# Kernel optimization log

Measured on AMD Instinct MI355X. Metric: run time of the kernel, lower is better.

Reference implementation:

```python
import jax, jax.numpy as jnp
import numpy as np

TAU = 2.0        # LIF membrane time constant
VTH = 1.0        # firing threshold
ALPHA = 2.0      # ATan surrogate sharpness (spikingjelly default)
EPS = 1e-5       # LayerNorm eps


@jax.custom_vjp
def spike(x):
    # Heaviside forward, ATan surrogate backward (spikingjelly surrogate.ATan)
    return (x >= 0).astype(x.dtype)

def _spike_fwd(x):
    return (x >= 0).astype(x.dtype), x

def _spike_bwd(x, g):
    return (g * (ALPHA / 2.0) / (1.0 + (jnp.pi / 2.0 * ALPHA * x) ** 2),)

spike.defvjp(_spike_fwd, _spike_bwd)


def lif(x_tbd):
    """Multi-step LIF neuron, decay_input=True, hard reset v_reset=0, detach_reset=True.
    x_tbd: [T, B, D] -> spikes [T, B, D]."""
    def step(v, x):
        v = v + (x - v) / TAU                       # leaky integrate
        s = spike(v - VTH)                          # fire
        v = v * (1.0 - jax.lax.stop_gradient(s))    # detached hard reset to 0
        return v, s
    v0 = jnp.zeros(x_tbd.shape[1:], x_tbd.dtype)
    _, s = jax.lax.scan(step, v0, x_tbd)
    return s


def layernorm(x, g, b):
    m = x.mean(-1, keepdims=True)
    v = ((x - m) ** 2).mean(-1, keepdims=True)
    return (x - m) * jax.lax.rsqrt(v + EPS) * g + b


def setup_inputs() -> dict:
    key = jax.random.key(0)
    ks = jax.random.split(key, 8)
    B, T, IN, H0, D, HD, DEPTH = 64, 2048, 4, 64, 128, 256, 4
    def w(k, shape, fan_in):
        return jax.random.normal(k, shape, jnp.float32) * (1.0 / np.sqrt(fan_in))
    return {
        "hist_feat": jax.random.normal(ks[0], (B, T, IN), jnp.float32),
        # projector params
        "pw1": w(ks[1], (IN, H0), IN), "pb1": jnp.zeros((H0,), jnp.float32),
        "pw2": w(ks[2], (H0, D), H0), "pb2": jnp.zeros((D,), jnp.float32),
        # stacked block params [DEPTH, ...]
        "fc1_w": w(ks[3], (DEPTH, D, HD), D), "fc1_b": jnp.zeros((DEPTH, HD), jnp.float32),
        "n1_g": jnp.ones((DEPTH, HD), jnp.float32), "n1_b": jnp.zeros((DEPTH, HD), jnp.float32),
        "fc2_w": w(ks[4], (DEPTH, HD, D), HD), "fc2_b": jnp.zeros((DEPTH, D), jnp.float32),
        "n2_g": jnp.ones((DEPTH, D), jnp.float32), "n2_b": jnp.zeros((DEPTH, D), jnp.float32),
    }


def reference(hist_feat, pw1, pb1, pw2, pb2, fc1_w, fc1_b, n1_g, n1_b,
              fc2_w, fc2_b, n2_g, n2_b):
    # SpikeInputProjector: Linear -> exact GELU -> Linear
    x = jax.nn.gelu(hist_feat @ pw1 + pb1, approximate=False) @ pw2 + pb2  # [B,T,D]
    depth = fc1_w.shape[0]
    for i in range(depth):  # small fixed structural loop over blocks
        r = x
        h = layernorm(x @ fc1_w[i] + fc1_b[i], n1_g[i], n1_b[i])   # [B,T,HD]
        h = lif(h.swapaxes(0, 1)).swapaxes(0, 1)                    # LIF over time
        h = layernorm(h @ fc2_w[i] + fc2_b[i], n2_g[i], n2_b[i])   # [B,T,D]
        h = lif(h.swapaxes(0, 1)).swapaxes(0, 1)
        x = r + h
    return x[:, -1]  # pooling='last', mask=None
```

## Files before the change

kernel.cpp:

```cpp
#include <hip/hip_runtime.h>
#include <math.h>

#define NB   64
#define TT   2048
#define TW   64
#define T0   (TT - TW)
#define NR   (NB * TW)

typedef float v2f __attribute__((ext_vector_type(2)));

__device__ __forceinline__ float gelu_exact(float x) {
    return 0.5f * x * (1.0f + erff(x * 0.7071067811865476f));
}
__device__ __forceinline__ unsigned long long rfl64(unsigned long long x) {
    unsigned lo = __builtin_amdgcn_readfirstlane((unsigned)x);
    unsigned hi = __builtin_amdgcn_readfirstlane((unsigned)(x >> 32));
    return ((unsigned long long)hi << 32) | lo;
}

#define XT_O   0
#define WB0_O  4096
#define WB1_O  12288
#define V1_O   20480
#define V2_O   20736
#define MSK_O  20864
#define LB_TOT 21120

__global__ void __launch_bounds__(512) fused_kernel(
    const float* __restrict__ hist,
    const float* __restrict__ pw1, const float* __restrict__ pb1,
    const float* __restrict__ pw2, const float* __restrict__ pb2,
    const float* __restrict__ fc1w, const float* __restrict__ fc1b,
    const float* __restrict__ n1g,  const float* __restrict__ n1b,
    const float* __restrict__ fc2w, const float* __restrict__ fc2b,
    const float* __restrict__ n2g,  const float* __restrict__ n2b,
    float* __restrict__ v1buf, float* __restrict__ v2buf,
    int* __restrict__ flg1, int* __restrict__ flg2,
    float* __restrict__ out)
{
    __shared__ __align__(16) float LB[LB_TOT];
    __shared__ int FLG[2];
    unsigned long long* MSK = (unsigned long long*)&LB[MSK_O];
    const int tid = threadIdx.x, wave = tid >> 6, lane = tid & 63;
    const int b = blockIdx.x & 63, half = blockIdx.x >> 6;
    const int row0 = wave * 4;

    if (tid == 0) { FLG[0] = 0; FLG[1] = 0; }

    float4 ra, rb, rc, rd;
#define LOADQ(src) { const float4* p_ = (const float4*)(src); \
                     ra = p_[tid]; rb = p_[tid+512]; rc = p_[tid+1024]; rd = p_[tid+1536]; }
#define WRITEQ(off) { float4* q_ = (float4*)&LB[off]; \
                      q_[tid] = ra; q_[tid+512] = rb; q_[tid+1024] = rc; q_[tid+1536] = rd; }
#define CONSUME(WOFF, KQ) \
    { \
        _Pragma("unroll 2") \
        for (int k4 = 0; k4 < 8; ++k4) { \
            float4 xr[4]; \
            _Pragma("unroll") \
            for (int r = 0; r < 4; ++r) \
                xr[r] = *(const float4*)&LB[XT_O + (row0+r)*128 + (KQ) + k4*4]; \
            _Pragma("unroll") \
            for (int kk = 0; kk < 4; ++kk) { \
                float4 wv = ((const float4*)&LB[(WOFF) + (k4*4+kk)*256])[lane]; \
                v2f wA, wB; wA.x = wv.x; wA.y = wv.y; wB.x = wv.z; wB.y = wv.w; \
                _Pragma("unroll") \
                for (int r = 0; r < 4; ++r) { \
                    float xv = ((const float*)&xr[r])[kk]; \
                    accA[r] += wA * xv; \
                    accB[r] += wB * xv; \
                } \
            } \
        } \
    }

    LOADQ(fc1w);

    {
        const float* hb = hist + ((size_t)b * TT + T0 + half*32) * 4;
        float w0 = pw1[lane], w1 = pw1[64+lane], w2 = pw1[128+lane], w3 = pw1[192+lane];
        float bb = pb1[lane];
        #pragma unroll
        for (int r = 0; r < 4; ++r) {
            int t = row0 + r;
            float4 h = *(const float4*)(hb + t*4);
            LB[WB1_O + t*64 + lane] = gelu_exact(bb + h.x*w0 + h.y*w1 + h.z*w2 + h.w*w3);
        }
    }
    WRITEQ(WB0_O);
    LOADQ(fc1w + 8192);
    {
        float2 bv = ((const float2*)pb2)[lane];
        v2f acc[4];
        #pragma unroll
        for (int r = 0; r < 4; ++r) { acc[r].x = 0.f; acc[r].y = 0.f; }
        #pragma unroll 2
        for (int k4 = 0; k4 < 16; ++k4) {
            float4 xr[4];
            #pragma unroll
            for (int r = 0; r < 4; ++r)
                xr[r] = *(const float4*)&LB[WB1_O + (row0+r)*64 + k4*4];
            #pragma unroll
            for (int kk = 0; kk < 4; ++kk) {
                v2f w = ((const v2f*)(pw2 + (k4*4+kk)*128))[lane];
                #pragma unroll
                for (int r = 0; r < 4; ++r) {
                    float xv = ((const float*)&xr[r])[kk];
                    acc[r] += w * xv;
                }
            }
        }
        #pragma unroll
        for (int r = 0; r < 4; ++r) {
            float2 o; o.x = acc[r].x + bv.x; o.y = acc[r].y + bv.y;
            *(float2*)&LB[XT_O + (row0+r)*128 + lane*2] = o;
        }
    }

    #pragma unroll 1
    for (int l = 0; l < 4; ++l) {
        const float* W1l = fc1w + (size_t)l * 32768;
        const float* W1n = fc1w + (size_t)(l < 3 ? l+1 : l) * 32768;
        const float* W2g = fc2w + (size_t)l * 32768;

        v2f accA[4], accB[4];
        #pragma unroll
        for (int r = 0; r < 4; ++r) {
            accA[r].x = 0.f; accA[r].y = 0.f;
            accB[r].x = 0.f; accB[r].y = 0.f;
        }
        __syncthreads(); WRITEQ(WB1_O); LOADQ(W1l + 16384); CONSUME(WB0_O, 0);
        __syncthreads(); WRITEQ(WB0_O); LOADQ(W1l + 24576); CONSUME(WB1_O, 32);
        __syncthreads(); WRITEQ(WB1_O); LOADQ(W1n);         CONSUME(WB0_O, 64);
        __syncthreads(); WRITEQ(WB0_O); LOADQ(W1n + 8192);  CONSUME(WB1_O, 96);

        {
            float4 b1v = ((const float4*)(fc1b + l*256))[lane];
            float4 g1v = ((const float4*)(n1g  + l*256))[lane];
            float4 t1v = ((const float4*)(n1b  + l*256))[lane];
            #pragma unroll
            for (int r = 0; r < 4; ++r) {
                float a0 = accA[r].x + b1v.x, a1 = accA[r].y + b1v.y;
                float a2 = accB[r].x + b1v.z, a3 = accB[r].y + b1v.w;
                float s = a0 + a1 + a2 + a3;
                #pragma unroll
                for (int m = 1; m < 64; m <<= 1) s += __shfl_xor(s, m, 64);
                float mean = s * (1.0f/256.0f);
                float dx = a0-mean, dy = a1-mean, dz = a2-mean, dw = a3-mean;
                float q2 = dx*dx + dy*dy + dz*dz + dw*dw;
                #pragma unroll
                for (int m = 1; m < 64; m <<= 1) q2 += __shfl_xor(q2, m, 64);
                float inv = 1.0f / sqrtf(q2 * (1.0f/256.0f) + 1e-5f);
                accA[r].x = dx*inv*g1v.x + t1v.x; accA[r].y = dy*inv*g1v.y + t1v.y;
                accB[r].x = dz*inv*g1v.z + t1v.z; accB[r].y = dw*inv*g1v.w + t1v.w;
            }
        }
        {
            const int tgt = l*8 + wave;
            while (__hip_atomic_load(&FLG[0], __ATOMIC_ACQUIRE,
                                     __HIP_MEMORY_SCOPE_WORKGROUP) < tgt)
                __builtin_amdgcn_s_sleep(1);
            float v0, v1, v2, v3;
            if (wave == 0) {
                if (half == 0) { v0 = v1 = v2 = v3 = 0.f; }
                else {
                    while (__hip_atomic_load(&flg1[b], __ATOMIC_RELAXED,
                                             __HIP_MEMORY_SCOPE_AGENT) < l+1)
                        __builtin_amdgcn_s_sleep(1);
                    __builtin_amdgcn_fence(__ATOMIC_ACQUIRE, "agent");
                    float4 vv = *(const float4*)&v1buf[(size_t)l*NB*256 + b*256 + lane*4];
                    v0 = vv.x; v1 = vv.y; v2 = vv.z; v3 = vv.w;
                }
            } else {
                float4 vv = *(const float4*)&LB[V1_O + lane*4];
                v0 = vv.x; v1 = vv.y; v2 = vv.z; v3 = vv.w;
            }
            #pragma unroll
            for (int i = 0; i < 4; ++i) {
                v0 += (accA[i].x - v0) * 0.5f;
                v1 += (accA[i].y - v1) * 0.5f;
                v2 += (accB[i].x - v2) * 0.5f;
                v3 += (accB[i].y - v3) * 0.5f;
                bool s0 = v0 >= 1.f, s1 = v1 >= 1.f, s2 = v2 >= 1.f, s3 = v3 >= 1.f;
                unsigned long long b0 = __ballot(s0), b1 = __ballot(s1);
                unsigned long long b2 = __ballot(s2), b3 = __ballot(s3);
                if (lane == 0) {
                    unsigned long long* mp = MSK + (size_t)(wave*4 + i)*4;
                    mp[0] = b0; mp[1] = b1; mp[2] = b2; mp[3] = b3;
                }
                v0 = s0 ? 0.f : v0;  v1 = s1 ? 0.f : v1;
                v2 = s2 ? 0.f : v2;  v3 = s3 ? 0.f : v3;
            }
            if (wave < 7) {
                float4 vv; vv.x = v0; vv.y = v1; vv.z = v2; vv.w = v3;
                *(float4*)&LB[V1_O + lane*4] = vv;
            } else if (half == 0) {
                float4 vv; vv.x = v0; vv.y = v1; vv.z = v2; vv.w = v3;
                *(float4*)&v1buf[(size_t)l*NB*256 + b*256 + lane*4] = vv;
                __builtin_amdgcn_fence(__ATOMIC_RELEASE, "agent");
                if (lane == 0)
                    __hip_atomic_store(&flg1[b], l+1, __ATOMIC_RELAXED,
                                       __HIP_MEMORY_SCOPE_AGENT);
            }
            if (lane == 0)
                __hip_atomic_store(&FLG[0], tgt+1, __ATOMIC_RELEASE,
                                   __HIP_MEMORY_SCOPE_WORKGROUP);
        }
        float a2x[4], a2y[4];
        #pragma unroll
        for (int i = 0; i < 4; ++i) {
            const unsigned long long* mp = MSK + (size_t)(wave*4 + i)*4;
            unsigned long long m0 = rfl64(mp[0]);
            unsigned long long m1 = rfl64(mp[1]);
            unsigned long long m2 = rfl64(mp[2]);
            unsigned long long m3 = rfl64(mp[3]);
            unsigned long long mm = m0 | m1 | m2 | m3;
            float ax = 0.f, ay = 0.f;
            if (mm) {
                int id = __builtin_ctzll(mm); mm &= mm - 1;
                const float* wr = W2g + (size_t)id * 512;
                float2 w0 = ((const float2*)(wr      ))[lane];
                float2 w1 = ((const float2*)(wr + 128))[lane];
                float2 w2 = ((const float2*)(wr + 256))[lane];
                float2 w3 = ((const float2*)(wr + 384))[lane];
                unsigned long long bit = 1ull << id;
                while (mm) {
                    int id2 = __builtin_ctzll(mm); mm &= mm - 1;
                    const float* wr2 = W2g + (size_t)id2 * 512;
                    float2 n0 = ((const float2*)(wr2      ))[lane];
                    float2 n1 = ((const float2*)(wr2 + 128))[lane];
                    float2 n2 = ((const float2*)(wr2 + 256))[lane];
                    float2 n3 = ((const float2*)(wr2 + 384))[lane];
                    ax += (m0 & bit) ? w0.x : 0.f;  ay += (m0 & bit) ? w0.y : 0.f;
                    ax += (m1 & bit) ? w1.x : 0.f;  ay += (m1 & bit) ? w1.y : 0.f;
                    ax += (m2 & bit) ? w2.x : 0.f;  ay += (m2 & bit) ? w2.y : 0.f;
                    ax += (m3 & bit) ? w3.x : 0.f;  ay += (m3 & bit) ? w3.y : 0.f;
                    bit = 1ull << id2;
                    w0 = n0; w1 = n1; w2 = n2; w3 = n3;
                }
                ax += (m0 & bit) ? w0.x : 0.f;  ay += (m0 & bit) ? w0.y : 0.f;
                ax += (m1 & bit) ? w1.x : 0.f;  ay += (m1 & bit) ? w1.y : 0.f;
                ax += (m2 & bit) ? w2.x : 0.f;  ay += (m2 & bit) ? w2.y : 0.f;
                ax += (m3 & bit) ? w3.x : 0.f;  ay += (m3 & bit) ? w3.y : 0.f;
            }
            a2x[i] = ax; a2y[i] = ay;
        }
        {
            float2 b2v = ((const float2*)(fc2b + l*128))[lane];
            float2 g2v = ((const float2*)(n2g  + l*128))[lane];
            float2 t2v = ((const float2*)(n2b  + l*128))[lane];
            #pragma unroll
            for (int i = 0; i < 4; ++i) {
                float ax = a2x[i] + b2v.x, ay = a2y[i] + b2v.y;
                float s = ax + ay;
                #pragma unroll
                for (int m = 1; m < 64; m <<= 1) s += __shfl_xor(s, m, 64);
                float mean = s * (1.0f/128.0f);
                float dx = ax - mean, dy = ay - mean;
                float q = dx*dx + dy*dy;
                #pragma unroll
                for (int m = 1; m < 64; m <<= 1) q += __shfl_xor(q, m, 64);
                float inv = 1.0f / sqrtf(q * (1.0f/128.0f) + 1e-5f);
                a2x[i] = dx*inv*g2v.x + t2v.x;
                a2y[i] = dy*inv*g2v.y + t2v.y;
            }
        }
        {
            const int tgt = l*8 + wave;
            while (__hip_atomic_load(&FLG[1], __ATOMIC_ACQUIRE,
                                     __HIP_MEMORY_SCOPE_WORKGROUP) < tgt)
                __builtin_amdgcn_s_sleep(1);
            float u0, u1;
            if (wave == 0) {
                if (half == 0) { u0 = u1 = 0.f; }
                else {
                    while (__hip_atomic_load(&flg2[b], __ATOMIC_RELAXED,
                                             __HIP_MEMORY_SCOPE_AGENT) < l+1)
                        __builtin_amdgcn_s_sleep(1);
                    __builtin_amdgcn_fence(__ATOMIC_ACQUIRE, "agent");
                    float2 uv = *(const float2*)&v2buf[(size_t)l*NB*128 + b*128 + lane*2];
                    u0 = uv.x; u1 = uv.y;
                }
            } else {
                float2 uv = *(const float2*)&LB[V2_O + lane*2];
                u0 = uv.x; u1 = uv.y;
            }
            #pragma unroll
            for (int i = 0; i < 4; ++i) {
                int t = row0 + i;
                u0 += (a2x[i] - u0) * 0.5f;
                u1 += (a2y[i] - u1) * 0.5f;
                bool s0 = u0 >= 1.f, s1 = u1 >= 1.f;
                float2 xv = *(const float2*)&LB[XT_O + t*128 + lane*2];
                float2 xn;
                xn.x = xv.x + (s0 ? 1.f : 0.f);
                xn.y = xv.y + (s1 ? 1.f : 0.f);
                *(float2*)&LB[XT_O + t*128 + lane*2] = xn;
                u0 = s0 ? 0.f : u0;
                u1 = s1 ? 0.f : u1;
                if (l == 3 && half == 1 && t == 31)
                    ((float2*)(out + b*128))[lane] = xn;
            }
            if (wave < 7) {
                float2 uv; uv.x = u0; uv.y = u1;
                *(float2*)&LB[V2_O + lane*2] = uv;
            } else if (half == 0) {
                float2 uv; uv.x = u0; uv.y = u1;
                *(float2*)&v2buf[(size_t)l*NB*128 + b*128 + lane*2] = uv;
                __builtin_amdgcn_fence(__ATOMIC_RELEASE, "agent");
                if (lane == 0)
                    __hip_atomic_store(&flg2[b], l+1, __ATOMIC_RELAXED,
                                       __HIP_MEMORY_SCOPE_AGENT);
            }
            if (lane == 0)
                __hip_atomic_store(&FLG[1], tgt+1, __ATOMIC_RELEASE,
                                   __HIP_MEMORY_SCOPE_WORKGROUP);
        }
    }
#undef LOADQ
#undef WRITEQ
#undef CONSUME
}

extern "C" void kernel_launch(void* const* d_in, const int* in_sizes, int n_in,
                              void* d_out, int out_size, void* d_ws, size_t ws_size,
                              hipStream_t stream) {
    const float* hist = (const float*)d_in[0];
    const float* pw1  = (const float*)d_in[1];
    const float* pb1  = (const float*)d_in[2];
    const float* pw2  = (const float*)d_in[3];
    const float* pb2  = (const float*)d_in[4];
    const float* fc1w = (const float*)d_in[5];
    const float* fc1b = (const float*)d_in[6];
    const float* n1g  = (const float*)d_in[7];
    const float* n1b  = (const float*)d_in[8];
    const float* fc2w = (const float*)d_in[9];
    const float* fc2b = (const float*)d_in[10];
    const float* n2g  = (const float*)d_in[11];
    const float* n2b  = (const float*)d_in[12];
    float* out = (float*)d_out;

    char* ws = (char*)d_ws;
    float* v1buf = (float*)ws;
    float* v2buf = (float*)(ws + (1ull << 20));
    int*   flg1  = (int*)(ws + (2ull << 20));
    int*   flg2  = flg1 + 64;

    hipMemsetAsync(flg1, 0, 128 * sizeof(int), stream);
    fused_kernel<<<128, 512, 0, stream>>>(hist, pw1, pb1, pw2, pb2,
                                          fc1w, fc1b, n1g, n1b,
                                          fc2w, fc2b, n2g, n2b,
                                          v1buf, v2buf, flg1, flg2, out);
}
```

Measured before the change: 198.3 us.

## Replace sparse spike-driven fc2 gather with dense LDS-staged matmul over spike bitmasks

The fc2 product was computed by walking the set bits of the spike masks and fetching the matching weight rows from global memory, which gives data-dependent loops and scattered uncached loads. It now streams fc2 weights through the existing double-buffered LDS pipeline and runs a dense FMA loop, multiplying each weight by a 0/1 value taken from the ballot masks held in registers. This also drops the LDS mask buffer and the readfirstlane round trip. The cost is dense work even when few neurons spike, plus four more barrier stages per layer.

```diff
diff --git a/kernel.cpp b/kernel.cpp
--- a/kernel.cpp
+++ b/kernel.cpp
@@ -12,19 +12,13 @@
 __device__ __forceinline__ float gelu_exact(float x) {
     return 0.5f * x * (1.0f + erff(x * 0.7071067811865476f));
 }
-__device__ __forceinline__ unsigned long long rfl64(unsigned long long x) {
-    unsigned lo = __builtin_amdgcn_readfirstlane((unsigned)x);
-    unsigned hi = __builtin_amdgcn_readfirstlane((unsigned)(x >> 32));
-    return ((unsigned long long)hi << 32) | lo;
-}
 
 #define XT_O   0
 #define WB0_O  4096
 #define WB1_O  12288
 #define V1_O   20480
 #define V2_O   20736
-#define MSK_O  20864
-#define LB_TOT 21120
+#define LB_TOT 20864
 
 __global__ void __launch_bounds__(512) fused_kernel(
     const float* __restrict__ hist,
@@ -40,7 +34,6 @@
 {
     __shared__ __align__(16) float LB[LB_TOT];
     __shared__ int FLG[2];
-    unsigned long long* MSK = (unsigned long long*)&LB[MSK_O];
     const int tid = threadIdx.x, wave = tid >> 6, lane = tid & 63;
     const int b = blockIdx.x & 63, half = blockIdx.x >> 6;
     const int row0 = wave * 4;
@@ -73,6 +66,23 @@
             } \
         } \
     }
+#define CONSUME2(WOFF, JB) \
+    { \
+        _Pragma("unroll 2") \
+        for (int k4 = 0; k4 < 16; ++k4) { \
+            const unsigned sh = (JB) + k4; \
+            _Pragma("unroll") \
+            for (int kk = 0; kk < 4; ++kk) { \
+                float2 wv = ((const float2*)&LB[(WOFF) + (k4*4+kk)*128])[lane]; \
+                v2f wp; wp.x = wv.x; wp.y = wv.y; \
+                _Pragma("unroll") \
+                for (int i = 0; i < 4; ++i) { \
+                    float xv = (float)((Mk[kk][i] >> sh) & 1ull); \
+                    acc2[i] += wp * xv; \
+                } \
+            } \
+        } \
+    }
 
     LOADQ(fc1w);
 
@@ -131,8 +141,8 @@
         }
         __syncthreads(); WRITEQ(WB1_O); LOADQ(W1l + 16384); CONSUME(WB0_O, 0);
         __syncthreads(); WRITEQ(WB0_O); LOADQ(W1l + 24576); CONSUME(WB1_O, 32);
-        __syncthreads(); WRITEQ(WB1_O); LOADQ(W1n);         CONSUME(WB0_O, 64);
-        __syncthreads(); WRITEQ(WB0_O); LOADQ(W1n + 8192);  CONSUME(WB1_O, 96);
+        __syncthreads(); WRITEQ(WB1_O); LOADQ(W2g);         CONSUME(WB0_O, 64);
+        __syncthreads(); WRITEQ(WB0_O); LOADQ(W2g + 8192);  CONSUME(WB1_O, 96);
 
         {
             float4 b1v = ((const float4*)(fc1b + l*256))[lane];
@@ -155,6 +165,7 @@
                 accB[r].x = dz*inv*g1v.z + t1v.z; accB[r].y = dw*inv*g1v.w + t1v.w;
             }
         }
+        unsigned long long Mk[4][4];
         {
             const int tgt = l*8 + wave;
             while (__hip_atomic_load(&FLG[0], __ATOMIC_ACQUIRE,
@@ -182,12 +193,8 @@
                 v2 += (accB[i].x - v2) * 0.5f;
                 v3 += (accB[i].y - v3) * 0.5f;
                 bool s0 = v0 >= 1.f, s1 = v1 >= 1.f, s2 = v2 >= 1.f, s3 = v3 >= 1.f;
-                unsigned long long b0 = __ballot(s0), b1 = __ballot(s1);
-                unsigned long long b2 = __ballot(s2), b3 = __ballot(s3);
-                if (lane == 0) {
-                    unsigned long long* mp = MSK + (size_t)(wave*4 + i)*4;
-                    mp[0] = b0; mp[1] = b1; mp[2] = b2; mp[3] = b3;
-                }
+                Mk[0][i] = __ballot(s0); Mk[1][i] = __ballot(s1);
+                Mk[2][i] = __ballot(s2); Mk[3][i] = __ballot(s3);
                 v0 = s0 ? 0.f : v0;  v1 = s1 ? 0.f : v1;
                 v2 = s2 ? 0.f : v2;  v3 = s3 ? 0.f : v3;
             }
@@ -206,52 +213,21 @@
                 __hip_atomic_store(&FLG[0], tgt+1, __ATOMIC_RELEASE,
                                    __HIP_MEMORY_SCOPE_WORKGROUP);
         }
-        float a2x[4], a2y[4];
-        #pragma unroll
-        for (int i = 0; i < 4; ++i) {
-            const unsigned long long* mp = MSK + (size_t)(wave*4 + i)*4;
-            unsigned long long m0 = rfl64(mp[0]);
-            unsigned long long m1 = rfl64(mp[1]);
-            unsigned long long m2 = rfl64(mp[2]);
-            unsigned long long m3 = rfl64(mp[3]);
-            unsigned long long mm = m0 | m1 | m2 | m3;
-            float ax = 0.f, ay = 0.f;
-            if (mm) {
-                int id = __builtin_ctzll(mm); mm &= mm - 1;
-                const float* wr = W2g + (size_t)id * 512;
-                float2 w0 = ((const float2*)(wr      ))[lane];
-                float2 w1 = ((const float2*)(wr + 128))[lane];
-                float2 w2 = ((const float2*)(wr + 256))[lane];
-                float2 w3 = ((const float2*)(wr + 384))[lane];
-                unsigned long long bit = 1ull << id;
-                while (mm) {
-                    int id2 = __builtin_ctzll(mm); mm &= mm - 1;
-                    const float* wr2 = W2g + (size_t)id2 * 512;
-                    float2 n0 = ((const float2*)(wr2      ))[lane];
-                    float2 n1 = ((const float2*)(wr2 + 128))[lane];
-                    float2 n2 = ((const float2*)(wr2 + 256))[lane];
-                    float2 n3 = ((const float2*)(wr2 + 384))[lane];
-                    ax += (m0 & bit) ? w0.x : 0.f;  ay += (m0 & bit) ? w0.y : 0.f;
-                    ax += (m1 & bit) ? w1.x : 0.f;  ay += (m1 & bit) ? w1.y : 0.f;
-                    ax += (m2 & bit) ? w2.x : 0.f;  ay += (m2 & bit) ? w2.y : 0.f;
-                    ax += (m3 & bit) ? w3.x : 0.f;  ay += (m3 & bit) ? w3.y : 0.f;
-                    bit = 1ull << id2;
-                    w0 = n0; w1 = n1; w2 = n2; w3 = n3;
-                }
-                ax += (m0 & bit) ? w0.x : 0.f;  ay += (m0 & bit) ? w0.y : 0.f;
-                ax += (m1 & bit) ? w1.x : 0.f;  ay += (m1 & bit) ? w1.y : 0.f;
-                ax += (m2 & bit) ? w2.x : 0.f;  ay += (m2 & bit) ? w2.y : 0.f;
-                ax += (m3 & bit) ? w3.x : 0.f;  ay += (m3 & bit) ? w3.y : 0.f;
-            }
-            a2x[i] = ax; a2y[i] = ay;
-        }
+        v2f acc2[4];
+        #pragma unroll
+        for (int i = 0; i < 4; ++i) { acc2[i].x = 0.f; acc2[i].y = 0.f; }
+        __syncthreads(); WRITEQ(WB1_O); LOADQ(W2g + 16384); CONSUME2(WB0_O, 0);
+        __syncthreads(); WRITEQ(WB0_O); LOADQ(W2g + 24576); CONSUME2(WB1_O, 16);
+        __syncthreads(); WRITEQ(WB1_O); LOADQ(W1n);         CONSUME2(WB0_O, 32);
+        __syncthreads(); WRITEQ(WB0_O); LOADQ(W1n + 8192);  CONSUME2(WB1_O, 48);
+
         {
             float2 b2v = ((const float2*)(fc2b + l*128))[lane];
             float2 g2v = ((const float2*)(n2g  + l*128))[lane];
             float2 t2v = ((const float2*)(n2b  + l*128))[lane];
             #pragma unroll
             for (int i = 0; i < 4; ++i) {
-                float ax = a2x[i] + b2v.x, ay = a2y[i] + b2v.y;
+                float ax = acc2[i].x + b2v.x, ay = acc2[i].y + b2v.y;
                 float s = ax + ay;
                 #pragma unroll
                 for (int m = 1; m < 64; m <<= 1) s += __shfl_xor(s, m, 64);
@@ -261,8 +237,8 @@
                 #pragma unroll
                 for (int m = 1; m < 64; m <<= 1) q += __shfl_xor(q, m, 64);
                 float inv = 1.0f / sqrtf(q * (1.0f/128.0f) + 1e-5f);
-                a2x[i] = dx*inv*g2v.x + t2v.x;
-                a2y[i] = dy*inv*g2v.y + t2v.y;
+                acc2[i].x = dx*inv*g2v.x + t2v.x;
+                acc2[i].y = dy*inv*g2v.y + t2v.y;
             }
         }
         {
@@ -288,8 +264,8 @@
             #pragma unroll
             for (int i = 0; i < 4; ++i) {
                 int t = row0 + i;
-                u0 += (a2x[i] - u0) * 0.5f;
-                u1 += (a2y[i] - u1) * 0.5f;
+                u0 += (acc2[i].x - u0) * 0.5f;
+                u1 += (acc2[i].y - u1) * 0.5f;
                 bool s0 = u0 >= 1.f, s1 = u1 >= 1.f;
                 float2 xv = *(const float2*)&LB[XT_O + t*128 + lane*2];
                 float2 xn;
@@ -320,6 +296,7 @@
 #undef LOADQ
 #undef WRITEQ
 #undef CONSUME
+#undef CONSUME2
 }
 
 extern "C" void kernel_launch(void* const* d_in, const int* in_sizes, int n_in,
```

After: 252.9 us. 27.6% more time.

## Double fc1 weight chunk size, keep spike masks in registers, batch sparse gathers

Applied to the files above, without the earlier changes.

The fc1 weights are now staged in two 64-row chunks per layer instead of four 32-row chunks. This halves the number of block barriers and LDS refill rounds but doubles the staging registers and LDS footprint. Spike ballot masks now stay in registers instead of going through LDS with readfirstlane, which removes LDS traffic. The sparse fc2 gather loop is restructured to issue four weight rows' loads at a time for more memory-level parallelism, at the cost of higher register pressure that may reduce occupancy.

```diff
diff --git a/kernel.cpp b/kernel.cpp
--- a/kernel.cpp
+++ b/kernel.cpp
@@ -12,19 +12,13 @@
 __device__ __forceinline__ float gelu_exact(float x) {
     return 0.5f * x * (1.0f + erff(x * 0.7071067811865476f));
 }
-__device__ __forceinline__ unsigned long long rfl64(unsigned long long x) {
-    unsigned lo = __builtin_amdgcn_readfirstlane((unsigned)x);
-    unsigned hi = __builtin_amdgcn_readfirstlane((unsigned)(x >> 32));
-    return ((unsigned long long)hi << 32) | lo;
-}
 
 #define XT_O   0
 #define WB0_O  4096
-#define WB1_O  12288
-#define V1_O   20480
-#define V2_O   20736
-#define MSK_O  20864
-#define LB_TOT 21120
+#define WB1_O  20480
+#define V1_O   36864
+#define V2_O   37120
+#define LB_TOT 37248
 
 __global__ void __launch_bounds__(512) fused_kernel(
     const float* __restrict__ hist,
@@ -40,22 +34,27 @@
 {
     __shared__ __align__(16) float LB[LB_TOT];
     __shared__ int FLG[2];
-    unsigned long long* MSK = (unsigned long long*)&LB[MSK_O];
     const int tid = threadIdx.x, wave = tid >> 6, lane = tid & 63;
     const int b = blockIdx.x & 63, half = blockIdx.x >> 6;
     const int row0 = wave * 4;
 
     if (tid == 0) { FLG[0] = 0; FLG[1] = 0; }
 
-    float4 ra, rb, rc, rd;
+    float4 r0, r1, r2, r3, r4, r5, r6, r7;
 #define LOADQ(src) { const float4* p_ = (const float4*)(src); \
-                     ra = p_[tid]; rb = p_[tid+512]; rc = p_[tid+1024]; rd = p_[tid+1536]; }
+                     r0 = p_[tid];        r1 = p_[tid + 512]; \
+                     r2 = p_[tid + 1024]; r3 = p_[tid + 1536]; \
+                     r4 = p_[tid + 2048]; r5 = p_[tid + 2560]; \
+                     r6 = p_[tid + 3072]; r7 = p_[tid + 3584]; }
 #define WRITEQ(off) { float4* q_ = (float4*)&LB[off]; \
-                      q_[tid] = ra; q_[tid+512] = rb; q_[tid+1024] = rc; q_[tid+1536] = rd; }
+                      q_[tid]        = r0; q_[tid + 512]  = r1; \
+                      q_[tid + 1024] = r2; q_[tid + 1536] = r3; \
+                      q_[tid + 2048] = r4; q_[tid + 2560] = r5; \
+                      q_[tid + 3072] = r6; q_[tid + 3584] = r7; }
 #define CONSUME(WOFF, KQ) \
     { \
         _Pragma("unroll 2") \
-        for (int k4 = 0; k4 < 8; ++k4) { \
+        for (int k4 = 0; k4 < 16; ++k4) { \
             float4 xr[4]; \
             _Pragma("unroll") \
             for (int r = 0; r < 4; ++r) \
@@ -88,7 +87,7 @@
         }
     }
     WRITEQ(WB0_O);
-    LOADQ(fc1w + 8192);
+    LOADQ(fc1w + 16384);
     {
         float2 bv = ((const float2*)pb2)[lane];
         v2f acc[4];
@@ -119,7 +118,6 @@
 
     #pragma unroll 1
     for (int l = 0; l < 4; ++l) {
-        const float* W1l = fc1w + (size_t)l * 32768;
         const float* W1n = fc1w + (size_t)(l < 3 ? l+1 : l) * 32768;
         const float* W2g = fc2w + (size_t)l * 32768;
 
@@ -129,10 +127,8 @@
             accA[r].x = 0.f; accA[r].y = 0.f;
             accB[r].x = 0.f; accB[r].y = 0.f;
         }
-        __syncthreads(); WRITEQ(WB1_O); LOADQ(W1l + 16384); CONSUME(WB0_O, 0);
-        __syncthreads(); WRITEQ(WB0_O); LOADQ(W1l + 24576); CONSUME(WB1_O, 32);
-        __syncthreads(); WRITEQ(WB1_O); LOADQ(W1n);         CONSUME(WB0_O, 64);
-        __syncthreads(); WRITEQ(WB0_O); LOADQ(W1n + 8192);  CONSUME(WB1_O, 96);
+        __syncthreads(); WRITEQ(WB1_O); LOADQ(W1n);          CONSUME(WB0_O, 0);
+        __syncthreads(); WRITEQ(WB0_O); LOADQ(W1n + 16384);  CONSUME(WB1_O, 64);
 
         {
             float4 b1v = ((const float4*)(fc1b + l*256))[lane];
@@ -155,6 +151,7 @@
                 accB[r].x = dz*inv*g1v.z + t1v.z; accB[r].y = dw*inv*g1v.w + t1v.w;
             }
         }
+        unsigned long long Mk[4][4];
         {
             const int tgt = l*8 + wave;
             while (__hip_atomic_load(&FLG[0], __ATOMIC_ACQUIRE,
@@ -182,12 +179,8 @@
                 v2 += (accB[i].x - v2) * 0.5f;
                 v3 += (accB[i].y - v3) * 0.5f;
                 bool s0 = v0 >= 1.f, s1 = v1 >= 1.f, s2 = v2 >= 1.f, s3 = v3 >= 1.f;
-                unsigned long long b0 = __ballot(s0), b1 = __ballot(s1);
-                unsigned long long b2 = __ballot(s2), b3 = __ballot(s3);
-                if (lane == 0) {
-                    unsigned long long* mp = MSK + (size_t)(wave*4 + i)*4;
-                    mp[0] = b0; mp[1] = b1; mp[2] = b2; mp[3] = b3;
-                }
+                Mk[0][i] = __ballot(s0); Mk[1][i] = __ballot(s1);
+                Mk[2][i] = __ballot(s2); Mk[3][i] = __ballot(s3);
                 v0 = s0 ? 0.f : v0;  v1 = s1 ? 0.f : v1;
                 v2 = s2 ? 0.f : v2;  v3 = s3 ? 0.f : v3;
             }
@@ -209,14 +202,56 @@
         float a2x[4], a2y[4];
         #pragma unroll
         for (int i = 0; i < 4; ++i) {
-            const unsigned long long* mp = MSK + (size_t)(wave*4 + i)*4;
-            unsigned long long m0 = rfl64(mp[0]);
-            unsigned long long m1 = rfl64(mp[1]);
-            unsigned long long m2 = rfl64(mp[2]);
-            unsigned long long m3 = rfl64(mp[3]);
+            unsigned long long m0 = Mk[0][i], m1 = Mk[1][i];
+            unsigned long long m2 = Mk[2][i], m3 = Mk[3][i];
             unsigned long long mm = m0 | m1 | m2 | m3;
             float ax = 0.f, ay = 0.f;
-            if (mm) {
+            int ng = __popcll(mm) >> 2;
+            for (int g = 0; g < ng; ++g) {
+                int i0 = __builtin_ctzll(mm); mm &= mm - 1;
+                int i1 = __builtin_ctzll(mm); mm &= mm - 1;
+                int i2 = __builtin_ctzll(mm); mm &= mm - 1;
+                int i3 = __builtin_ctzll(mm); mm &= mm - 1;
+                const float* p0 = W2g + (size_t)i0 * 512;
+                const float* p1 = W2g + (size_t)i1 * 512;
+                const float* p2 = W2g + (size_t)i2 * 512;
+                const float* p3 = W2g + (size_t)i3 * 512;
+                float2 w00 = ((const float2*)(p0      ))[lane];
+                float2 w01 = ((const float2*)(p0 + 128))[lane];
+                float2 w02 = ((const float2*)(p0 + 256))[lane];
+                float2 w03 = ((const float2*)(p0 + 384))[lane];
+                float2 w10 = ((const float2*)(p1      ))[lane];
+                float2 w11 = ((const float2*)(p1 + 128))[lane];
+                float2 w12 = ((const float2*)(p1 + 256))[lane];
+                float2 w13 = ((const float2*)(p1 + 384))[lane];
+                float2 w20 = ((const float2*)(p2      ))[lane];
+                float2 w21 = ((const float2*)(p2 + 128))[lane];
+                float2 w22 = ((const float2*)(p2 + 256))[lane];
+                float2 w23 = ((const float2*)(p2 + 384))[lane];
+                float2 w30 = ((const float2*)(p3      ))[lane];
+                float2 w31 = ((const float2*)(p3 + 128))[lane];
+                float2 w32 = ((const float2*)(p3 + 256))[lane];
+                float2 w33 = ((const float2*)(p3 + 384))[lane];
+                unsigned long long b0 = 1ull << i0, b1 = 1ull << i1;
+                unsigned long long b2 = 1ull << i2, b3 = 1ull << i3;
+                ax += (m0 & b0) ? w00.x : 0.f;  ay += (m0 & b0) ? w00.y : 0.f;
+                ax += (m1 & b0) ? w01.x : 0.f;  ay += (m1 & b0) ? w01.y : 0.f;
+                ax += (m2 & b0) ? w02.x : 0.f;  ay += (m2 & b0) ? w02.y : 0.f;
+                ax += (m3 & b0) ? w03.x : 0.f;  ay += (m3 & b0) ? w03.y : 0.f;
+                ax += (m0 & b1) ? w10.x : 0.f;  ay += (m0 & b1) ? w10.y : 0.f;
+                ax += (m1 & b1) ? w11.x : 0.f;  ay += (m1 & b1) ? w11.y : 0.f;
+                ax += (m2 & b1) ? w12.x : 0.f;  ay += (m2 & b1) ? w12.y : 0.f;
+                ax += (m3 & b1) ? w13.x : 0.f;  ay += (m3 & b1) ? w13.y : 0.f;
+                ax += (m0 & b2) ? w20.x : 0.f;  ay += (m0 & b2) ? w20.y : 0.f;
+                ax += (m1 & b2) ? w21.x : 0.f;  ay += (m1 & b2) ? w21.y : 0.f;
+                ax += (m2 & b2) ? w22.x : 0.f;  ay += (m2 & b2) ? w22.y : 0.f;
+                ax += (m3 & b2) ? w23.x : 0.f;  ay += (m3 & b2) ? w23.y : 0.f;
+                ax += (m0 & b3) ? w30.x : 0.f;  ay += (m0 & b3) ? w30.y : 0.f;
+                ax += (m1 & b3) ? w31.x : 0.f;  ay += (m1 & b3) ? w31.y : 0.f;
+                ax += (m2 & b3) ? w32.x : 0.f;  ay += (m2 & b3) ? w32.y : 0.f;
+                ax += (m3 & b3) ? w33.x : 0.f;  ay += (m3 & b3) ? w33.y : 0.f;
+            }
+            while (mm) {
                 int id = __builtin_ctzll(mm); mm &= mm - 1;
                 const float* wr = W2g + (size_t)id * 512;
                 float2 w0 = ((const float2*)(wr      ))[lane];
@@ -224,20 +259,6 @@
                 float2 w2 = ((const float2*)(wr + 256))[lane];
                 float2 w3 = ((const float2*)(wr + 384))[lane];
                 unsigned long long bit = 1ull << id;
-                while (mm) {
-                    int id2 = __builtin_ctzll(mm); mm &= mm - 1;
-                    const float* wr2 = W2g + (size_t)id2 * 512;
-                    float2 n0 = ((const float2*)(wr2      ))[lane];
-                    float2 n1 = ((const float2*)(wr2 + 128))[lane];
-                    float2 n2 = ((const float2*)(wr2 + 256))[lane];
-                    float2 n3 = ((const float2*)(wr2 + 384))[lane];
-                    ax += (m0 & bit) ? w0.x : 0.f;  ay += (m0 & bit) ? w0.y : 0.f;
-                    ax += (m1 & bit) ? w1.x : 0.f;  ay += (m1 & bit) ? w1.y : 0.f;
-                    ax += (m2 & bit) ? w2.x : 0.f;  ay += (m2 & bit) ? w2.y : 0.f;
-                    ax += (m3 & bit) ? w3.x : 0.f;  ay += (m3 & bit) ? w3.y : 0.f;
-                    bit = 1ull << id2;
-                    w0 = n0; w1 = n1; w2 = n2; w3 = n3;
-                }
                 ax += (m0 & bit) ? w0.x : 0.f;  ay += (m0 & bit) ? w0.y : 0.f;
                 ax += (m1 & bit) ? w1.x : 0.f;  ay += (m1 & bit) ? w1.y : 0.f;
                 ax += (m2 & bit) ? w2.x : 0.f;  ay += (m2 & bit) ? w2.y : 0.f;
```

Result: faster. 182.5 us (-7.9%).
